# Kernel optimization log

Measured on AMD Instinct MI355X. Metric: run time of the kernel, lower is better.

Reference implementation:

```python
import jax, jax.numpy as jnp
import numpy as np

INP_DIM = 1024
PROJ_DIM = 1024
SEQ = 2048
BATCH = 4

def setup_inputs() -> dict:
    key = jax.random.key(0)
    k1, k2, k3, k4 = jax.random.split(key, 4)
    inputs = jax.random.normal(k1, (BATCH, SEQ, INP_DIM), dtype=jnp.float32)
    # nn.Linear weights stored as (out, in); we keep them that way and transpose in matmul
    Wq = jax.random.normal(k2, (PROJ_DIM, INP_DIM), dtype=jnp.float32) * (1.0 / np.sqrt(INP_DIM))
    Wk = jax.random.normal(k3, (PROJ_DIM, INP_DIM), dtype=jnp.float32) * (1.0 / np.sqrt(INP_DIM))
    Wv = jax.random.normal(k4, (PROJ_DIM, INP_DIM), dtype=jnp.float32) * (1.0 / np.sqrt(INP_DIM))
    return {"inputs": inputs, "Wq": Wq, "Wk": Wk, "Wv": Wv}

def reference(inputs, Wq, Wk, Wv):
    # QKV projections: x @ W.T (nn.Linear convention)
    Q = jnp.einsum('bsd,pd->bsp', inputs, Wq)
    K = jnp.einsum('bsd,pd->bsp', inputs, Wk)
    V = jnp.einsum('bsd,pd->bsp', inputs, Wv)
    scores = jnp.einsum('bqp,bkp->bqk', Q, K)  # [B, S, S]
    n = inputs.shape[1]
    causal = jnp.tril(jnp.ones((n, n), dtype=bool))  # True = keep
    scores = jnp.where(causal, scores, -jnp.inf)
    weights = jax.nn.softmax(scores / jnp.sqrt(jnp.float32(Q.shape[-1])), axis=-1)
    # dropout rate = 0.0 -> identity
    Z = jnp.einsum('bqk,bkp->bqp', weights, V)
    return Z
```

## Files before the change

### kernel.cpp

```cpp
#include <hip/hip_runtime.h>
#include <stdint.h>

#define SEQ   2048
#define DIM   1024
#define BATCH 4

typedef _Float16 f16;
typedef __attribute__((ext_vector_type(8))) _Float16 f16x8;
typedef __attribute__((ext_vector_type(4))) _Float16 f16x4;
typedef __attribute__((ext_vector_type(4))) float   f32x4;

typedef void __attribute__((address_space(1))) vg_t;
typedef void __attribute__((address_space(3))) vl_t;

__device__ __forceinline__ void gld16(const void* g, void* l) {
  __builtin_amdgcn_global_load_lds((vg_t*)g, (vl_t*)l, 16, 0, 0);
}

__global__ __launch_bounds__(256) void cvt_all(const float* __restrict__ x,
                                               const float* __restrict__ wq,
                                               const float* __restrict__ wk,
                                               const float* __restrict__ wv,
                                               f16* __restrict__ xb,
                                               f16* __restrict__ wh) {
  const int bx = blockIdx.x;
  const float* in; f16* out; int base;
  if (bx < 8192)       { in = x;  out = xb;             base = bx; }
  else if (bx < 9216)  { in = wq; out = wh;             base = bx - 8192; }
  else if (bx < 10240) { in = wk; out = wh + (1 << 20); base = bx - 9216; }
  else                 { in = wv; out = wh + (2 << 20); base = bx - 10240; }
  const long i = ((long)base * 256 + threadIdx.x) * 4;
  float4 v = *(const float4*)(in + i);
  f16x4 o = { (f16)v.x, (f16)v.y, (f16)v.z, (f16)v.w };
  *(f16x4*)(out + i) = o;
}

template <int MODE, int CAUSAL>
__global__ __launch_bounds__(256) void gemm_bt(const f16* __restrict__ A, int lda, long aOffZ,
                                               const f16* __restrict__ B, int ldb, long bOffZ,
                                               void* __restrict__ Cv, int ldc, long cOffZ,
                                               int K) {
  constexpr int BK = 64;
  __shared__ __align__(16) f16 lA[2][128 * BK];
  __shared__ __align__(16) f16 lB[2][128 * BK];

  const int tid  = threadIdx.x;
  const int wave = tid >> 6;
  const int lane = tid & 63;
  const int m0 = blockIdx.x * 128;
  const int n0 = blockIdx.y * 128;
  const int z  = blockIdx.z;

  if (CAUSAL == 1 && n0 >= m0 + 128) return;
  const int Keff = (CAUSAL == 2) ? (m0 + 128) : K;

  const f16* Ab = A + (long)z * aOffZ + (long)m0 * lda;
  const f16* Bb = B + (long)z * bOffZ + (long)n0 * ldb;

  const int wm = (wave & 1) * 64;
  const int wn = (wave >> 1) * 64;

  f32x4 acc[4][4] = {};

  const int srow = lane >> 3;
  const int sj   = lane & 7;
  const int fr   = lane & 15;
  const int fq   = lane >> 4;

  auto stage = [&](int buf, int kt) {
#pragma unroll
    for (int j = 0; j < 4; ++j) {
      const int rgrp = j * 4 + wave;
      const int row  = rgrp * 8 + srow;
      const int gch  = sj ^ (row & 7);
      gld16(Ab + (long)row * lda + kt + gch * 8, (void*)(&lA[buf][rgrp * 512 + lane * 8]));
      gld16(Bb + (long)row * ldb + kt + gch * 8, (void*)(&lB[buf][rgrp * 512 + lane * 8]));
    }
  };

  auto compute = [&](int buf) {
#pragma unroll
    for (int kk = 0; kk < BK; kk += 32) {
      f16x8 af[4], bf[4];
#pragma unroll
      for (int i = 0; i < 4; ++i) {
        const int arow = wm + i * 16 + fr;
        const int ach  = (kk / 8 + fq) ^ (arow & 7);
        af[i] = *(const f16x8*)(&lA[buf][arow * BK + ach * 8]);
        const int brow = wn + i * 16 + fr;
        const int bch  = (kk / 8 + fq) ^ (brow & 7);
        bf[i] = *(const f16x8*)(&lB[buf][brow * BK + bch * 8]);
      }
#pragma unroll
      for (int mi = 0; mi < 4; ++mi)
#pragma unroll
        for (int ni = 0; ni < 4; ++ni)
          acc[mi][ni] = __builtin_amdgcn_mfma_f32_16x16x32_f16(af[mi], bf[ni], acc[mi][ni], 0, 0, 0);
    }
  };

  stage(0, 0);
  for (int kt = 0; kt < Keff; kt += 2 * BK) {
    __syncthreads();
    if (kt + BK < Keff) stage(1, kt + BK);
    compute(0);
    if (kt + BK < Keff) {
      __syncthreads();
      if (kt + 2 * BK < Keff) stage(0, kt + 2 * BK);
      compute(1);
    }
  }

#pragma unroll
  for (int mi = 0; mi < 4; ++mi) {
    const int row = m0 + wm + mi * 16 + fq * 4;
#pragma unroll
    for (int ni = 0; ni < 4; ++ni) {
      const int col = n0 + wn + ni * 16 + fr;
      if constexpr (MODE == 0) {
        float* C = (float*)Cv + (long)z * cOffZ;
#pragma unroll
        for (int r = 0; r < 4; ++r) C[(long)(row + r) * ldc + col] = acc[mi][ni][r];
      } else if constexpr (MODE == 1) {
        f16* C = (f16*)Cv + (long)z * cOffZ;
#pragma unroll
        for (int r = 0; r < 4; ++r) C[(long)(row + r) * ldc + col] = (f16)acc[mi][ni][r];
      } else if constexpr (MODE == 2) {
        f16* C = (f16*)Cv + (long)z * cOffZ;
        f16x4 o = { (f16)acc[mi][ni][0], (f16)acc[mi][ni][1],
                    (f16)acc[mi][ni][2], (f16)acc[mi][ni][3] };
        *(f16x4*)(C + (long)col * ldc + row) = o;
      } else {
        f16* Qh  = (f16*)Cv;
        f16* Kh  = Qh + (size_t)8 * 1024 * 1024;
        f16* VTb = Kh + (size_t)8 * 1024 * 1024;
        if (col < 1024) {
#pragma unroll
          for (int r = 0; r < 4; ++r) Qh[(long)(row + r) * DIM + col] = (f16)acc[mi][ni][r];
        } else if (col < 2048) {
#pragma unroll
          for (int r = 0; r < 4; ++r) Kh[(long)(row + r) * DIM + (col - 1024)] = (f16)acc[mi][ni][r];
        } else {
          f16x4 o = { (f16)acc[mi][ni][0], (f16)acc[mi][ni][1],
                      (f16)acc[mi][ni][2], (f16)acc[mi][ni][3] };
          *(f16x4*)(VTb + (long)(col - 2048) * (BATCH * SEQ) + row) = o;
        }
      }
    }
  }
}

__global__ __launch_bounds__(256) void softmax_causal(f16* S) {
  const int q = blockIdx.x, b = blockIdx.y;
  f16* row = S + ((long)b * SEQ + q) * SEQ;
  const int tid = threadIdx.x;
  const int lane = tid & 63, wave = tid >> 6;
  const int nvalid = q + 1;

  f16x8 vv = *(const f16x8*)(row + tid * 8);
  float v[8];
  float m = -3.0e38f;
#pragma unroll
  for (int i = 0; i < 8; ++i) {
    const int k = tid * 8 + i;
    v[i] = (k < nvalid) ? (float)vv[i] * 0.03125f : -3.0e38f;
    m = fmaxf(m, v[i]);
  }
#pragma unroll
  for (int off = 32; off; off >>= 1) m = fmaxf(m, __shfl_xor(m, off));
  __shared__ float redm[4], reds[4];
  if (lane == 0) redm[wave] = m;
  __syncthreads();
  m = fmaxf(fmaxf(redm[0], redm[1]), fmaxf(redm[2], redm[3]));

  float s = 0.f;
#pragma unroll
  for (int i = 0; i < 8; ++i) {
    const float p = (v[i] > -1.0e37f) ? __expf(v[i] - m) : 0.f;
    v[i] = p;
    s += p;
  }
#pragma unroll
  for (int off = 32; off; off >>= 1) s += __shfl_xor(s, off);
  if (lane == 0) reds[wave] = s;
  __syncthreads();
  s = reds[0] + reds[1] + reds[2] + reds[3];
  const float inv = 1.f / s;
  f16x8 o;
#pragma unroll
  for (int i = 0; i < 8; ++i) o[i] = (f16)(v[i] * inv);
  *(f16x8*)(row + tid * 8) = o;
}

extern "C" void kernel_launch(void* const* d_in, const int* in_sizes, int n_in,
                              void* d_out, int out_size, void* d_ws, size_t ws_size,
                              hipStream_t stream) {
  const float* x  = (const float*)d_in[0];
  const float* Wq = (const float*)d_in[1];
  const float* Wk = (const float*)d_in[2];
  const float* Wv = (const float*)d_in[3];
  float* out = (float*)d_out;

  if (ws_size < (size_t)51 * 1024 * 1024 * 2) return;

  f16* xb = (f16*)d_ws;
  f16* Wh = xb + (size_t)8 * 1024 * 1024;
  f16* Qh = Wh + (size_t)3 * 1024 * 1024;
  f16* Kh = Qh + (size_t)8 * 1024 * 1024;
  f16* VT = Kh + (size_t)8 * 1024 * 1024;
  f16* Sc = VT + (size_t)8 * 1024 * 1024;

  const long QOFF = (long)SEQ * DIM;
  const long SOFF = (long)SEQ * SEQ;

  cvt_all<<<11264, 256, 0, stream>>>(x, Wq, Wk, Wv, xb, Wh);

  gemm_bt<3, 0><<<dim3(64, 24, 1), 256, 0, stream>>>(xb, DIM, 0, Wh, DIM, 0, Qh, 0, 0, DIM);

  gemm_bt<1, 1><<<dim3(16, 16, 4), 256, 0, stream>>>(Qh, DIM, QOFF, Kh, DIM, QOFF,
                                                     Sc, SEQ, SOFF, DIM);

  softmax_causal<<<dim3(SEQ, BATCH), 256, 0, stream>>>(Sc);

  gemm_bt<0, 2><<<dim3(16, 8, 4), 256, 0, stream>>>(Sc, SEQ, SOFF,
                                                    VT, BATCH * SEQ, SEQ,
                                                    out, DIM, (long)SEQ * DIM, SEQ);
}
```

Measured before the change: 255.0 us.

## Launch only causal tiles for QK^T and reverse PV order, with BK=128 single buffer

The QK^T GEMM now launches exactly the 136 lower-triangular tiles per batch and maps a linear block index to (row, col) with a triangular-number inversion. This removes the many early-exit blocks of the old full grid. The PV GEMM reverses its m-tile order so the longest-K blocks are scheduled first, which is meant to reduce tail imbalance. Both attention GEMMs switch to a BK=128 single-buffered K loop with two barriers per step. That loses load/compute overlap in exchange for fewer iterations, and it keeps 64 KB of LDS, the same as the old double buffer.

```diff
diff --git a/kernel.cpp b/kernel.cpp
--- a/kernel.cpp
+++ b/kernel.cpp
@@ -1,5 +1,6 @@
 #include <hip/hip_runtime.h>
 #include <stdint.h>
+#include <math.h>
 
 #define SEQ   2048
 #define DIM   1024
@@ -35,23 +36,41 @@
   *(f16x4*)(out + i) = o;
 }
 
-template <int MODE, int CAUSAL>
+template <int MODE, int CAUSAL, int BK, int DBUF>
 __global__ __launch_bounds__(256) void gemm_bt(const f16* __restrict__ A, int lda, long aOffZ,
                                                const f16* __restrict__ B, int ldb, long bOffZ,
                                                void* __restrict__ Cv, int ldc, long cOffZ,
                                                int K) {
-  constexpr int BK = 64;
-  __shared__ __align__(16) f16 lA[2][128 * BK];
-  __shared__ __align__(16) f16 lB[2][128 * BK];
+  constexpr int CH  = BK / 8;
+  constexpr int RPL = 64 / CH;
+  constexpr int NL  = 32 / RPL;
+  constexpr int NB  = DBUF ? 2 : 1;
+  __shared__ __align__(16) f16 lA[NB][128 * BK];
+  __shared__ __align__(16) f16 lB[NB][128 * BK];
 
   const int tid  = threadIdx.x;
   const int wave = tid >> 6;
   const int lane = tid & 63;
-  const int m0 = blockIdx.x * 128;
-  const int n0 = blockIdx.y * 128;
-  const int z  = blockIdx.z;
-
-  if (CAUSAL == 1 && n0 >= m0 + 128) return;
+
+  int m0, n0, z;
+  if constexpr (CAUSAL == 3) {
+    const int bx = blockIdx.x;
+    z = bx / 136;
+    const int t2 = bx - z * 136;
+    int x = (int)((sqrtf(8.0f * (float)t2 + 1.0f) - 1.0f) * 0.5f);
+    while ((x + 1) * (x + 2) / 2 <= t2) ++x;
+    while (x * (x + 1) / 2 > t2) --x;
+    const int y = t2 - x * (x + 1) / 2;
+    m0 = x * 128; n0 = y * 128;
+  } else if constexpr (CAUSAL == 2) {
+    m0 = (int)(gridDim.x - 1 - blockIdx.x) * 128;
+    n0 = blockIdx.y * 128;
+    z  = blockIdx.z;
+  } else {
+    m0 = blockIdx.x * 128;
+    n0 = blockIdx.y * 128;
+    z  = blockIdx.z;
+  }
   const int Keff = (CAUSAL == 2) ? (m0 + 128) : K;
 
   const f16* Ab = A + (long)z * aOffZ + (long)m0 * lda;
@@ -62,17 +81,17 @@
 
   f32x4 acc[4][4] = {};
 
-  const int srow = lane >> 3;
-  const int sj   = lane & 7;
+  const int srow = lane / CH;
+  const int sj   = lane % CH;
   const int fr   = lane & 15;
   const int fq   = lane >> 4;
 
   auto stage = [&](int buf, int kt) {
 #pragma unroll
-    for (int j = 0; j < 4; ++j) {
+    for (int j = 0; j < NL; ++j) {
       const int rgrp = j * 4 + wave;
-      const int row  = rgrp * 8 + srow;
-      const int gch  = sj ^ (row & 7);
+      const int row  = rgrp * RPL + srow;
+      const int gch  = sj ^ (row & (CH - 1));
       gld16(Ab + (long)row * lda + kt + gch * 8, (void*)(&lA[buf][rgrp * 512 + lane * 8]));
       gld16(Bb + (long)row * ldb + kt + gch * 8, (void*)(&lB[buf][rgrp * 512 + lane * 8]));
     }
@@ -85,10 +104,10 @@
 #pragma unroll
       for (int i = 0; i < 4; ++i) {
         const int arow = wm + i * 16 + fr;
-        const int ach  = (kk / 8 + fq) ^ (arow & 7);
+        const int ach  = (kk / 8 + fq) ^ (arow & (CH - 1));
         af[i] = *(const f16x8*)(&lA[buf][arow * BK + ach * 8]);
         const int brow = wn + i * 16 + fr;
-        const int bch  = (kk / 8 + fq) ^ (brow & 7);
+        const int bch  = (kk / 8 + fq) ^ (brow & (CH - 1));
         bf[i] = *(const f16x8*)(&lB[buf][brow * BK + bch * 8]);
       }
 #pragma unroll
@@ -99,15 +118,24 @@
     }
   };
 
-  stage(0, 0);
-  for (int kt = 0; kt < Keff; kt += 2 * BK) {
-    __syncthreads();
-    if (kt + BK < Keff) stage(1, kt + BK);
-    compute(0);
-    if (kt + BK < Keff) {
+  if constexpr (DBUF) {
+    stage(0, 0);
+    for (int kt = 0; kt < Keff; kt += 2 * BK) {
       __syncthreads();
-      if (kt + 2 * BK < Keff) stage(0, kt + 2 * BK);
-      compute(1);
+      if (kt + BK < Keff) stage(1, kt + BK);
+      compute(0);
+      if (kt + BK < Keff) {
+        __syncthreads();
+        if (kt + 2 * BK < Keff) stage(0, kt + 2 * BK);
+        compute(1);
+      }
+    }
+  } else {
+    for (int kt = 0; kt < Keff; kt += BK) {
+      __syncthreads();
+      stage(0, kt);
+      __syncthreads();
+      compute(0);
     }
   }
 
@@ -215,14 +243,16 @@
 
   cvt_all<<<11264, 256, 0, stream>>>(x, Wq, Wk, Wv, xb, Wh);
 
-  gemm_bt<3, 0><<<dim3(64, 24, 1), 256, 0, stream>>>(xb, DIM, 0, Wh, DIM, 0, Qh, 0, 0, DIM);
-
-  gemm_bt<1, 1><<<dim3(16, 16, 4), 256, 0, stream>>>(Qh, DIM, QOFF, Kh, DIM, QOFF,
-                                                     Sc, SEQ, SOFF, DIM);
+  gemm_bt<3, 0, 64, 1><<<dim3(64, 24, 1), 256, 0, stream>>>(xb, DIM, 0, Wh, DIM, 0,
+                                                            Qh, 0, 0, DIM);
+
+  gemm_bt<1, 3, 128, 0><<<dim3(136 * BATCH, 1, 1), 256, 0, stream>>>(Qh, DIM, QOFF,
+                                                                     Kh, DIM, QOFF,
+                                                                     Sc, SEQ, SOFF, DIM);
 
   softmax_causal<<<dim3(SEQ, BATCH), 256, 0, stream>>>(Sc);
 
-  gemm_bt<0, 2><<<dim3(16, 8, 4), 256, 0, stream>>>(Sc, SEQ, SOFF,
-                                                    VT, BATCH * SEQ, SEQ,
-                                                    out, DIM, (long)SEQ * DIM, SEQ);
-}
+  gemm_bt<0, 2, 128, 0><<<dim3(16, 8, 4), 256, 0, stream>>>(Sc, SEQ, SOFF,
+                                                            VT, BATCH * SEQ, SEQ,
+                                                            out, DIM, (long)SEQ * DIM, SEQ);
+}
```

Result: no change. 253.0 us (-0.8%).
